# Performance work log

Measured on AMD Instinct MI355X. Metric: run time of the kernel, lower is better.

The kernel has to match this reference:

```python
import jax, jax.numpy as jnp
import numpy as np

B, N, D, H = 4, 2048, 512, 8
HEAD = D // H
TEMP = 8.0


def setup_inputs() -> dict:
    key = jax.random.key(0)
    k1, k2, k3, k4 = jax.random.split(key, 4)
    return {
        "keys": jax.random.normal(k1, (B, N, D), dtype=jnp.float32),
        "queries": jax.random.normal(k2, (B, N, D), dtype=jnp.float32),
        "values": jax.random.normal(k3, (B, N, D), dtype=jnp.float32),
        "W_comb": jax.random.normal(k4, (D, D), dtype=jnp.float32) * (1.0 / np.sqrt(D)),
        "b_comb": jnp.zeros((D,), dtype=jnp.float32),
    }


def reference(keys, queries, values, W_comb, b_comb):
    b, nk, d = keys.shape
    nq = queries.shape[1]
    h, hd = H, HEAD
    # split heads: (b, n, d) -> (b, n, h, hd)
    k = keys.reshape(b, nk, h, hd)
    q = queries.reshape(b, nq, h, hd)
    v = values.reshape(b, nk, h, hd)
    # scaled dot-product attention per head
    logits = jnp.einsum("bqhd,bkhd->bhqk", q, k) / TEMP  # (b, h, nq, nk)
    w = jax.nn.softmax(logits, axis=-1)
    out = jnp.einsum("bhqk,bkhd->bqhd", w, v).reshape(b, nq, d)
    # head_combine: Linear with bias (torch: x @ W.T + b)
    return out @ W_comb.T + b_comb
```

## Files before the change

kernel.cpp:

```cpp
#include <hip/hip_runtime.h>

#define B_ 4
#define N_ 2048
#define D_ 512
#define H_ 8

typedef __attribute__((ext_vector_type(8))) short bf16x8;
typedef __attribute__((ext_vector_type(4))) short bf16x4;
typedef __attribute__((ext_vector_type(4))) float f32x4;

#define KP 68

__device__ __forceinline__ unsigned short f32_to_bf16(float f) {
  unsigned int u = __float_as_uint(f);
  u += 0x7FFFu + ((u >> 16) & 1u);
  return (unsigned short)(u >> 16);
}

__device__ __forceinline__ unsigned int pack2_bf16(float a, float b) {
#if __has_builtin(__builtin_amdgcn_cvt_pk_bf16_f32)
  typedef __attribute__((ext_vector_type(2))) __bf16 bf16v2;
  bf16v2 r = __builtin_amdgcn_cvt_pk_bf16_f32(a, b);
  return *(unsigned int*)&r;
#else
  return (unsigned int)f32_to_bf16(a) | ((unsigned int)f32_to_bf16(b) << 16);
#endif
}

__device__ __forceinline__ float fast_exp2(float x) {
#if __has_builtin(__builtin_amdgcn_exp2f)
  return __builtin_amdgcn_exp2f(x);
#else
  return exp2f(x);
#endif
}

__device__ __forceinline__ f32x4 mfma16(bf16x4 a, bf16x4 b, f32x4 c) {
#if __has_builtin(__builtin_amdgcn_mfma_f32_16x16x16_bf16)
  return __builtin_amdgcn_mfma_f32_16x16x16_bf16(a, b, c, 0, 0, 0);
#else
  return __builtin_amdgcn_mfma_f32_16x16x16bf16_1k(a, b, c, 0, 0, 0);
#endif
}

__global__ __launch_bounds__(256) void convert_kernel(
    const float* __restrict__ Kf, const float* __restrict__ Qf,
    const float* __restrict__ Vf, const float* __restrict__ Wf,
    unsigned short* __restrict__ Qb, unsigned short* __restrict__ Kb,
    unsigned short* __restrict__ Wb, unsigned short* __restrict__ Vt) {
  __shared__ float tile[64 * 72];
  const int tid = threadIdx.x;
  if (blockIdx.x < 1024) {
    const float qs = 0.125f * 1.4426950408889634f;
    int gid = blockIdx.x * 256 + tid;
    const float4* Q4 = (const float4*)Qf;
    const float4* K4 = (const float4*)Kf;
    for (int i = gid; i < (B_ * N_ * D_) / 4; i += 262144) {
      float4 q = Q4[i];
      ((uint2*)Qb)[i] = make_uint2(pack2_bf16(q.x * qs, q.y * qs),
                                   pack2_bf16(q.z * qs, q.w * qs));
      float4 k = K4[i];
      ((uint2*)Kb)[i] = make_uint2(pack2_bf16(k.x, k.y), pack2_bf16(k.z, k.w));
    }
    if (gid < (D_ * D_) / 4) {
      float4 w = ((const float4*)Wf)[gid];
      ((uint2*)Wb)[gid] = make_uint2(pack2_bf16(w.x, w.y), pack2_bf16(w.z, w.w));
    }
  } else {
    int bid = blockIdx.x - 1024;
    int nt = bid & 31, bh = bid >> 5;
    int b = bh >> 3, h = bh & 7;
    int n0 = nt * 64;
#pragma unroll
    for (int i = 0; i < 4; ++i) {
      int idx = i * 256 + tid;
      int r = idx >> 4, c = idx & 15;
      *(float4*)&tile[r * 72 + c * 4] =
          *(const float4*)(Vf + (size_t)(b * N_ + n0 + r) * D_ + h * 64 + c * 4);
    }
    __syncthreads();
    int d = tid >> 2, c = tid & 3;
    unsigned int o[8];
#pragma unroll
    for (int j = 0; j < 8; ++j)
      o[j] = pack2_bf16(tile[(c * 16 + 2 * j) * 72 + d],
                        tile[(c * 16 + 2 * j + 1) * 72 + d]);
    unsigned short* dst = Vt + ((size_t)bh * 64 + d) * N_ + n0 + c * 16;
    *(bf16x8*)dst = *(bf16x8*)&o[0];
    *(bf16x8*)(dst + 8) = *(bf16x8*)&o[4];
  }
}

__global__ __launch_bounds__(256, 2) void attn_kernel(
    const unsigned short* __restrict__ Qb, const unsigned short* __restrict__ Kb,
    const unsigned short* __restrict__ Vt, unsigned short* __restrict__ Ob) {
  __shared__ unsigned short Kl[2][64 * KP];
  __shared__ unsigned short Vl[2][64 * KP];

  const int tid = threadIdx.x;
  const int w = tid >> 6;
  const int lane = tid & 63;
  const int lr = lane & 15;
  const int lq = lane >> 4;

  const int lid = blockIdx.y * gridDim.x + blockIdx.x;
  const int xcd = lid & 7;
  const int lin = lid >> 3;
  const int bh = xcd * 4 + (lin >> 4);
  const int qb = (lin & 15) * 128;

  const size_t slab = (size_t)(bh >> 3) * N_ * D_ + (size_t)(bh & 7) * 64;
  const unsigned short* kbase = Kb + slab;
  const unsigned short* vtbase = Vt + (size_t)bh * 64 * N_;

  bf16x8 qa[2][2];
#pragma unroll
  for (int g = 0; g < 2; ++g) {
    const unsigned short* qrow =
        Qb + slab + (size_t)(qb + w * 32 + g * 16 + lr) * D_;
    qa[g][0] = *(const bf16x8*)(qrow + 8 * lq);
    qa[g][1] = *(const bf16x8*)(qrow + 32 + 8 * lq);
  }

  f32x4 O[4][2];
#pragma unroll
  for (int i = 0; i < 4; ++i)
#pragma unroll
    for (int g = 0; g < 2; ++g) O[i][g] = (f32x4){0.f, 0.f, 0.f, 0.f};
  float l_g[2] = {0.f, 0.f};

  const int st_r = tid >> 3;
  const int st_c = tid & 7;

  {
    const unsigned short* ksrc = kbase + (size_t)st_r * D_ + st_c * 8;
    bf16x8 a = *(const bf16x8*)ksrc;
    bf16x8 b = *(const bf16x8*)(ksrc + (size_t)32 * D_);
    const unsigned short* vsrc = vtbase + (size_t)st_r * N_ + st_c * 8;
    bf16x8 c = *(const bf16x8*)vsrc;
    bf16x8 d = *(const bf16x8*)(vsrc + (size_t)32 * N_);
    *(bf16x8*)&Kl[0][st_r * KP + st_c * 8] = a;
    *(bf16x8*)&Kl[0][(st_r + 32) * KP + st_c * 8] = b;
    *(bf16x8*)&Vl[0][st_r * KP + st_c * 8] = c;
    *(bf16x8*)&Vl[0][(st_r + 32) * KP + st_c * 8] = d;
  }

  for (int kt = 0; kt < 32; ++kt) {
    const int p = kt & 1;
    __syncthreads();

    bf16x8 nk0, nk1, nv0, nv1;
    const bool more = (kt + 1) < 32;
    if (more) {
      const int kb1 = (kt + 1) * 64;
      const unsigned short* ksrc = kbase + (size_t)(kb1 + st_r) * D_ + st_c * 8;
      nk0 = *(const bf16x8*)ksrc;
      nk1 = *(const bf16x8*)(ksrc + (size_t)32 * D_);
      const unsigned short* vsrc = vtbase + (size_t)st_r * N_ + kb1 + st_c * 8;
      nv0 = *(const bf16x8*)vsrc;
      nv1 = *(const bf16x8*)(vsrc + (size_t)32 * N_);
    }

    f32x4 S[4][2];
#pragma unroll
    for (int nt = 0; nt < 4; ++nt) {
      bf16x8 kf0 = *(const bf16x8*)&Kl[p][(nt * 16 + lr) * KP + 8 * lq];
      bf16x8 kf1 = *(const bf16x8*)&Kl[p][(nt * 16 + lr) * KP + 32 + 8 * lq];
#pragma unroll
      for (int g = 0; g < 2; ++g) {
        S[nt][g] = __builtin_amdgcn_mfma_f32_16x16x32_bf16(
            kf0, qa[g][0], (f32x4){0.f, 0.f, 0.f, 0.f}, 0, 0, 0);
        S[nt][g] = __builtin_amdgcn_mfma_f32_16x16x32_bf16(kf1, qa[g][1],
                                                           S[nt][g], 0, 0, 0);
      }
    }

    bf16x4 pf[4][2];
#pragma unroll
    for (int nt = 0; nt < 4; ++nt)
#pragma unroll
      for (int g = 0; g < 2; ++g) {
        float p0 = fast_exp2(S[nt][g][0]);
        float p1 = fast_exp2(S[nt][g][1]);
        float p2 = fast_exp2(S[nt][g][2]);
        float p3 = fast_exp2(S[nt][g][3]);
        l_g[g] += (p0 + p1) + (p2 + p3);
        uint2 packed = make_uint2(pack2_bf16(p0, p1), pack2_bf16(p2, p3));
        pf[nt][g] = *(bf16x4*)&packed;
      }

#pragma unroll
    for (int dt = 0; dt < 4; ++dt) {
#pragma unroll
      for (int nt = 0; nt < 4; ++nt) {
        bf16x4 vf =
            *(const bf16x4*)&Vl[p][(dt * 16 + lr) * KP + nt * 16 + 4 * lq];
#pragma unroll
        for (int g = 0; g < 2; ++g)
          O[dt][g] = mfma16(vf, pf[nt][g], O[dt][g]);
      }
    }

    if (more) {
      *(bf16x8*)&Kl[1 - p][st_r * KP + st_c * 8] = nk0;
      *(bf16x8*)&Kl[1 - p][(st_r + 32) * KP + st_c * 8] = nk1;
      *(bf16x8*)&Vl[1 - p][st_r * KP + st_c * 8] = nv0;
      *(bf16x8*)&Vl[1 - p][(st_r + 32) * KP + st_c * 8] = nv1;
    }
  }

#pragma unroll
  for (int g = 0; g < 2; ++g) {
    l_g[g] += __shfl_xor(l_g[g], 16);
    l_g[g] += __shfl_xor(l_g[g], 32);
  }

  __syncthreads();
  unsigned short* SR = &Kl[0][0];
#pragma unroll
  for (int g = 0; g < 2; ++g) {
    float linv = 1.0f / l_g[g];
#pragma unroll
    for (int dt = 0; dt < 4; ++dt) {
      float v0 = O[dt][g][0] * linv;
      float v1 = O[dt][g][1] * linv;
      float v2 = O[dt][g][2] * linv;
      float v3 = O[dt][g][3] * linv;
      uint2 packed = make_uint2(pack2_bf16(v0, v1), pack2_bf16(v2, v3));
      *(bf16x4*)&SR[(w * 32 + g * 16 + lr) * KP + dt * 16 + lq * 4] =
          *(bf16x4*)&packed;
    }
  }
  __syncthreads();
  {
    const int row = tid >> 1, half = tid & 1;
    unsigned short* dst = Ob + slab + (size_t)(qb + row) * D_ + half * 32;
    const unsigned short* src = &SR[row * KP + half * 32];
    *(bf16x8*)dst = *(const bf16x8*)src;
    *(bf16x8*)(dst + 8) = *(const bf16x8*)(src + 8);
    *(bf16x8*)(dst + 16) = *(const bf16x8*)(src + 16);
    *(bf16x8*)(dst + 24) = *(const bf16x8*)(src + 24);
  }
}

#define GP 68
__global__ __launch_bounds__(256, 2) void gemm_kernel(
    const unsigned short* __restrict__ A, const unsigned short* __restrict__ Wb,
    const float* __restrict__ bias, float* __restrict__ out) {
  __shared__ unsigned short A_lds[2][64 * GP];
  __shared__ unsigned short W_lds[2][128 * GP];

  const int tid = threadIdx.x;
  const int w = tid >> 6;
  const int lane = tid & 63;
  const int lr = lane & 15;
  const int lq = lane >> 4;

  const int bid = blockIdx.x;
  const int xcd = bid & 7;
  const int lin = bid >> 3;
  const int mb = (xcd * 16 + (lin >> 2)) * 64;
  const int cb = (lin & 3) * 128;

  const int dc = (tid & 7) * 8;
  const int r0 = tid >> 3;

  f32x4 acc[8];
#pragma unroll
  for (int i = 0; i < 8; ++i) acc[i] = (f32x4){0.f, 0.f, 0.f, 0.f};

  {
    *(bf16x8*)&A_lds[0][r0 * GP + dc] =
        *(const bf16x8*)(A + (size_t)(mb + r0) * D_ + dc);
    *(bf16x8*)&A_lds[0][(r0 + 32) * GP + dc] =
        *(const bf16x8*)(A + (size_t)(mb + r0 + 32) * D_ + dc);
#pragma unroll
    for (int j = 0; j < 4; ++j)
      *(bf16x8*)&W_lds[0][(r0 + 32 * j) * GP + dc] =
          *(const bf16x8*)(Wb + (size_t)(cb + r0 + 32 * j) * D_ + dc);
  }

  for (int kt = 0; kt < 8; ++kt) {
    const int p = kt & 1;
    __syncthreads();

    bf16x8 na0, na1, nw0, nw1, nw2, nw3;
    const bool more = (kt + 1) < 8;
    if (more) {
      const int k1 = (kt + 1) * 64;
      na0 = *(const bf16x8*)(A + (size_t)(mb + r0) * D_ + k1 + dc);
      na1 = *(const bf16x8*)(A + (size_t)(mb + r0 + 32) * D_ + k1 + dc);
      nw0 = *(const bf16x8*)(Wb + (size_t)(cb + r0) * D_ + k1 + dc);
      nw1 = *(const bf16x8*)(Wb + (size_t)(cb + r0 + 32) * D_ + k1 + dc);
      nw2 = *(const bf16x8*)(Wb + (size_t)(cb + r0 + 64) * D_ + k1 + dc);
      nw3 = *(const bf16x8*)(Wb + (size_t)(cb + r0 + 96) * D_ + k1 + dc);
    }

    bf16x8 a0 = *(const bf16x8*)&A_lds[p][(w * 16 + lr) * GP + 8 * lq];
    bf16x8 a1 = *(const bf16x8*)&A_lds[p][(w * 16 + lr) * GP + 32 + 8 * lq];
#pragma unroll
    for (int nt = 0; nt < 8; ++nt) {
      bf16x8 b0 = *(const bf16x8*)&W_lds[p][(nt * 16 + lr) * GP + 8 * lq];
      bf16x8 b1 = *(const bf16x8*)&W_lds[p][(nt * 16 + lr) * GP + 32 + 8 * lq];
      acc[nt] = __builtin_amdgcn_mfma_f32_16x16x32_bf16(a0, b0, acc[nt], 0, 0, 0);
      acc[nt] = __builtin_amdgcn_mfma_f32_16x16x32_bf16(a1, b1, acc[nt], 0, 0, 0);
    }

    if (more) {
      *(bf16x8*)&A_lds[1 - p][r0 * GP + dc] = na0;
      *(bf16x8*)&A_lds[1 - p][(r0 + 32) * GP + dc] = na1;
      *(bf16x8*)&W_lds[1 - p][r0 * GP + dc] = nw0;
      *(bf16x8*)&W_lds[1 - p][(r0 + 32) * GP + dc] = nw1;
      *(bf16x8*)&W_lds[1 - p][(r0 + 64) * GP + dc] = nw2;
      *(bf16x8*)&W_lds[1 - p][(r0 + 96) * GP + dc] = nw3;
    }
  }

#pragma unroll
  for (int nt = 0; nt < 8; ++nt) {
    float bc = bias[cb + nt * 16 + lr];
#pragma unroll
    for (int rr = 0; rr < 4; ++rr) {
      int row = mb + w * 16 + lq * 4 + rr;
      out[(size_t)row * D_ + cb + nt * 16 + lr] = acc[nt][rr] + bc;
    }
  }
}

extern "C" void kernel_launch(void* const* d_in, const int* in_sizes, int n_in,
                              void* d_out, int out_size, void* d_ws,
                              size_t ws_size, hipStream_t stream) {
  (void)in_sizes; (void)n_in; (void)out_size; (void)ws_size;
  const float* keys    = (const float*)d_in[0];
  const float* queries = (const float*)d_in[1];
  const float* values  = (const float*)d_in[2];
  const float* W       = (const float*)d_in[3];
  const float* bias    = (const float*)d_in[4];
  float* out = (float*)d_out;

  char* ws = (char*)d_ws;
  unsigned short* Qb = (unsigned short*)(ws);
  unsigned short* Kb = (unsigned short*)(ws + 8388608);
  unsigned short* Vt = (unsigned short*)(ws + 16777216);
  unsigned short* Wb = (unsigned short*)(ws + 25165824);
  unsigned short* Ab = (unsigned short*)(ws + 25690112);

  convert_kernel<<<2048, 256, 0, stream>>>(keys, queries, values, W,
                                           Qb, Kb, Wb, Vt);

  attn_kernel<<<dim3(N_ / 128, B_ * H_), 256, 0, stream>>>(Qb, Kb, Vt, Ab);

  gemm_kernel<<<512, 256, 0, stream>>>(Ab, Wb, bias, out);
}
```

Before: 162.8 us.

## Fuse Q and W bf16 conversion into attention and GEMM kernels

Removes the separate Q and W fp32-to-bf16 conversion passes from the convert kernel. The attention kernel now loads fp32 queries and scales and converts them in registers, and the GEMM loads fp32 W tiles and converts them before storing to LDS. This cuts a full round trip of Q through the workspace, at the cost of wider fp32 loads in the consumers. The packing helper also drops the hardware packed-convert builtin in favour of software rounding.

Measured after the change: 163.7 us. Within noise of the previous version (+0.5%).

```diff
diff --git a/kernel.cpp b/kernel.cpp
--- a/kernel.cpp
+++ b/kernel.cpp
@@ -18,13 +18,16 @@
 }
 
 __device__ __forceinline__ unsigned int pack2_bf16(float a, float b) {
-#if __has_builtin(__builtin_amdgcn_cvt_pk_bf16_f32)
-  typedef __attribute__((ext_vector_type(2))) __bf16 bf16v2;
-  bf16v2 r = __builtin_amdgcn_cvt_pk_bf16_f32(a, b);
-  return *(unsigned int*)&r;
-#else
   return (unsigned int)f32_to_bf16(a) | ((unsigned int)f32_to_bf16(b) << 16);
-#endif
+}
+
+__device__ __forceinline__ bf16x8 cvt8_bf16(float4 a, float4 b, float s) {
+  union { unsigned int u[4]; bf16x8 v; } r;
+  r.u[0] = pack2_bf16(a.x * s, a.y * s);
+  r.u[1] = pack2_bf16(a.z * s, a.w * s);
+  r.u[2] = pack2_bf16(b.x * s, b.y * s);
+  r.u[3] = pack2_bf16(b.z * s, b.w * s);
+  return r.v;
 }
 
 __device__ __forceinline__ float fast_exp2(float x) {
@@ -44,27 +47,16 @@
 }
 
 __global__ __launch_bounds__(256) void convert_kernel(
-    const float* __restrict__ Kf, const float* __restrict__ Qf,
-    const float* __restrict__ Vf, const float* __restrict__ Wf,
-    unsigned short* __restrict__ Qb, unsigned short* __restrict__ Kb,
-    unsigned short* __restrict__ Wb, unsigned short* __restrict__ Vt) {
+    const float* __restrict__ Kf, const float* __restrict__ Vf,
+    unsigned short* __restrict__ Kb, unsigned short* __restrict__ Vt) {
   __shared__ float tile[64 * 72];
   const int tid = threadIdx.x;
   if (blockIdx.x < 1024) {
-    const float qs = 0.125f * 1.4426950408889634f;
     int gid = blockIdx.x * 256 + tid;
-    const float4* Q4 = (const float4*)Qf;
     const float4* K4 = (const float4*)Kf;
     for (int i = gid; i < (B_ * N_ * D_) / 4; i += 262144) {
-      float4 q = Q4[i];
-      ((uint2*)Qb)[i] = make_uint2(pack2_bf16(q.x * qs, q.y * qs),
-                                   pack2_bf16(q.z * qs, q.w * qs));
       float4 k = K4[i];
       ((uint2*)Kb)[i] = make_uint2(pack2_bf16(k.x, k.y), pack2_bf16(k.z, k.w));
-    }
-    if (gid < (D_ * D_) / 4) {
-      float4 w = ((const float4*)Wf)[gid];
-      ((uint2*)Wb)[gid] = make_uint2(pack2_bf16(w.x, w.y), pack2_bf16(w.z, w.w));
     }
   } else {
     int bid = blockIdx.x - 1024;
@@ -92,7 +84,7 @@
 }
 
 __global__ __launch_bounds__(256, 2) void attn_kernel(
-    const unsigned short* __restrict__ Qb, const unsigned short* __restrict__ Kb,
+    const float* __restrict__ Qf, const unsigned short* __restrict__ Kb,
     const unsigned short* __restrict__ Vt, unsigned short* __restrict__ Ob) {
   __shared__ unsigned short Kl[2][64 * KP];
   __shared__ unsigned short Vl[2][64 * KP];
@@ -114,12 +106,19 @@
   const unsigned short* vtbase = Vt + (size_t)bh * 64 * N_;
 
   bf16x8 qa[2][2];
-#pragma unroll
-  for (int g = 0; g < 2; ++g) {
-    const unsigned short* qrow =
-        Qb + slab + (size_t)(qb + w * 32 + g * 16 + lr) * D_;
-    qa[g][0] = *(const bf16x8*)(qrow + 8 * lq);
-    qa[g][1] = *(const bf16x8*)(qrow + 32 + 8 * lq);
+  {
+    const float qs = 0.125f * 1.4426950408889634f;
+#pragma unroll
+    for (int g = 0; g < 2; ++g) {
+      const float* qrow =
+          Qf + slab + (size_t)(qb + w * 32 + g * 16 + lr) * D_;
+      float4 a0 = *(const float4*)(qrow + 8 * lq);
+      float4 a1 = *(const float4*)(qrow + 8 * lq + 4);
+      qa[g][0] = cvt8_bf16(a0, a1, qs);
+      float4 b0 = *(const float4*)(qrow + 32 + 8 * lq);
+      float4 b1 = *(const float4*)(qrow + 36 + 8 * lq);
+      qa[g][1] = cvt8_bf16(b0, b1, qs);
+    }
   }
 
   f32x4 O[4][2];
@@ -245,7 +244,7 @@
 
 #define GP 68
 __global__ __launch_bounds__(256, 2) void gemm_kernel(
-    const unsigned short* __restrict__ A, const unsigned short* __restrict__ Wb,
+    const unsigned short* __restrict__ A, const float* __restrict__ Wf,
     const float* __restrict__ bias, float* __restrict__ out) {
   __shared__ unsigned short A_lds[2][64 * GP];
   __shared__ unsigned short W_lds[2][128 * GP];
@@ -275,25 +274,31 @@
     *(bf16x8*)&A_lds[0][(r0 + 32) * GP + dc] =
         *(const bf16x8*)(A + (size_t)(mb + r0 + 32) * D_ + dc);
 #pragma unroll
-    for (int j = 0; j < 4; ++j)
-      *(bf16x8*)&W_lds[0][(r0 + 32 * j) * GP + dc] =
-          *(const bf16x8*)(Wb + (size_t)(cb + r0 + 32 * j) * D_ + dc);
+    for (int j = 0; j < 4; ++j) {
+      const float* wsrc = Wf + (size_t)(cb + r0 + 32 * j) * D_ + dc;
+      float4 wa = *(const float4*)wsrc;
+      float4 wb = *(const float4*)(wsrc + 4);
+      *(bf16x8*)&W_lds[0][(r0 + 32 * j) * GP + dc] = cvt8_bf16(wa, wb, 1.0f);
+    }
   }
 
   for (int kt = 0; kt < 8; ++kt) {
     const int p = kt & 1;
     __syncthreads();
 
-    bf16x8 na0, na1, nw0, nw1, nw2, nw3;
+    bf16x8 na0, na1;
+    float4 nwA[4], nwB[4];
     const bool more = (kt + 1) < 8;
     if (more) {
       const int k1 = (kt + 1) * 64;
       na0 = *(const bf16x8*)(A + (size_t)(mb + r0) * D_ + k1 + dc);
       na1 = *(const bf16x8*)(A + (size_t)(mb + r0 + 32) * D_ + k1 + dc);
-      nw0 = *(const bf16x8*)(Wb + (size_t)(cb + r0) * D_ + k1 + dc);
-      nw1 = *(const bf16x8*)(Wb + (size_t)(cb + r0 + 32) * D_ + k1 + dc);
-      nw2 = *(const bf16x8*)(Wb + (size_t)(cb + r0 + 64) * D_ + k1 + dc);
-      nw3 = *(const bf16x8*)(Wb + (size_t)(cb + r0 + 96) * D_ + k1 + dc);
+#pragma unroll
+      for (int j = 0; j < 4; ++j) {
+        const float* wsrc = Wf + (size_t)(cb + r0 + 32 * j) * D_ + k1 + dc;
+        nwA[j] = *(const float4*)wsrc;
+        nwB[j] = *(const float4*)(wsrc + 4);
+      }
     }
 
     bf16x8 a0 = *(const bf16x8*)&A_lds[p][(w * 16 + lr) * GP + 8 * lq];
@@ -309,10 +314,10 @@
     if (more) {
       *(bf16x8*)&A_lds[1 - p][r0 * GP + dc] = na0;
       *(bf16x8*)&A_lds[1 - p][(r0 + 32) * GP + dc] = na1;
-      *(bf16x8*)&W_lds[1 - p][r0 * GP + dc] = nw0;
-      *(bf16x8*)&W_lds[1 - p][(r0 + 32) * GP + dc] = nw1;
-      *(bf16x8*)&W_lds[1 - p][(r0 + 64) * GP + dc] = nw2;
-      *(bf16x8*)&W_lds[1 - p][(r0 + 96) * GP + dc] = nw3;
+#pragma unroll
+      for (int j = 0; j < 4; ++j)
+        *(bf16x8*)&W_lds[1 - p][(r0 + 32 * j) * GP + dc] =
+            cvt8_bf16(nwA[j], nwB[j], 1.0f);
     }
   }
 
@@ -339,16 +344,13 @@
   float* out = (float*)d_out;
 
   char* ws = (char*)d_ws;
-  unsigned short* Qb = (unsigned short*)(ws);
   unsigned short* Kb = (unsigned short*)(ws + 8388608);
   unsigned short* Vt = (unsigned short*)(ws + 16777216);
-  unsigned short* Wb = (unsigned short*)(ws + 25165824);
   unsigned short* Ab = (unsigned short*)(ws + 25690112);
 
-  convert_kernel<<<2048, 256, 0, stream>>>(keys, queries, values, W,
-                                           Qb, Kb, Wb, Vt);
-
-  attn_kernel<<<dim3(N_ / 128, B_ * H_), 256, 0, stream>>>(Qb, Kb, Vt, Ab);
-
-  gemm_kernel<<<512, 256, 0, stream>>>(Ab, Wb, bias, out);
-}
+  convert_kernel<<<2048, 256, 0, stream>>>(keys, values, Kb, Vt);
+
+  attn_kernel<<<dim3(N_ / 128, B_ * H_), 256, 0, stream>>>(queries, Kb, Vt, Ab);
+
+  gemm_kernel<<<512, 256, 0, stream>>>(Ab, W, bias, out);
+}
```

## Halve attention block to two waves, each handling 64 query rows

Applied to the files above, without the earlier changes.

The attention kernel now launches 128 threads (two waves) per 128-query block instead of four. Each wave handles 64 query rows (four 16-row groups), so every K/V fragment read from LDS feeds twice as many MFMAs. Each thread now stages four rows of K and V per tile. The QK, exp and pack steps are also interleaved per group, which shortens the live range of the score registers. The trade-off is more registers per thread (larger O accumulators and Q fragments) and fewer waves per block to hide latency.

Result: slower. 201.6 us (+23.8%).

```diff
diff --git a/kernel.cpp b/kernel.cpp
--- a/kernel.cpp
+++ b/kernel.cpp
@@ -91,7 +91,7 @@
   }
 }
 
-__global__ __launch_bounds__(256, 2) void attn_kernel(
+__global__ __launch_bounds__(128, 2) void attn_kernel(
     const unsigned short* __restrict__ Qb, const unsigned short* __restrict__ Kb,
     const unsigned short* __restrict__ Vt, unsigned short* __restrict__ Ob) {
   __shared__ unsigned short Kl[2][64 * KP];
@@ -113,81 +113,71 @@
   const unsigned short* kbase = Kb + slab;
   const unsigned short* vtbase = Vt + (size_t)bh * 64 * N_;
 
-  bf16x8 qa[2][2];
-#pragma unroll
-  for (int g = 0; g < 2; ++g) {
+  bf16x8 qa[4][2];
+#pragma unroll
+  for (int g = 0; g < 4; ++g) {
     const unsigned short* qrow =
-        Qb + slab + (size_t)(qb + w * 32 + g * 16 + lr) * D_;
+        Qb + slab + (size_t)(qb + w * 64 + g * 16 + lr) * D_;
     qa[g][0] = *(const bf16x8*)(qrow + 8 * lq);
     qa[g][1] = *(const bf16x8*)(qrow + 32 + 8 * lq);
   }
 
-  f32x4 O[4][2];
+  f32x4 O[4][4];
 #pragma unroll
   for (int i = 0; i < 4; ++i)
 #pragma unroll
-    for (int g = 0; g < 2; ++g) O[i][g] = (f32x4){0.f, 0.f, 0.f, 0.f};
-  float l_g[2] = {0.f, 0.f};
+    for (int g = 0; g < 4; ++g) O[i][g] = (f32x4){0.f, 0.f, 0.f, 0.f};
+  float l_g[4] = {0.f, 0.f, 0.f, 0.f};
 
   const int st_r = tid >> 3;
   const int st_c = tid & 7;
 
   {
-    const unsigned short* ksrc = kbase + (size_t)st_r * D_ + st_c * 8;
-    bf16x8 a = *(const bf16x8*)ksrc;
-    bf16x8 b = *(const bf16x8*)(ksrc + (size_t)32 * D_);
-    const unsigned short* vsrc = vtbase + (size_t)st_r * N_ + st_c * 8;
-    bf16x8 c = *(const bf16x8*)vsrc;
-    bf16x8 d = *(const bf16x8*)(vsrc + (size_t)32 * N_);
-    *(bf16x8*)&Kl[0][st_r * KP + st_c * 8] = a;
-    *(bf16x8*)&Kl[0][(st_r + 32) * KP + st_c * 8] = b;
-    *(bf16x8*)&Vl[0][st_r * KP + st_c * 8] = c;
-    *(bf16x8*)&Vl[0][(st_r + 32) * KP + st_c * 8] = d;
+#pragma unroll
+    for (int j = 0; j < 4; ++j) {
+      const int r = st_r + 16 * j;
+      bf16x8 a = *(const bf16x8*)(kbase + (size_t)r * D_ + st_c * 8);
+      bf16x8 c = *(const bf16x8*)(vtbase + (size_t)r * N_ + st_c * 8);
+      *(bf16x8*)&Kl[0][r * KP + st_c * 8] = a;
+      *(bf16x8*)&Vl[0][r * KP + st_c * 8] = c;
+    }
   }
 
   for (int kt = 0; kt < 32; ++kt) {
     const int p = kt & 1;
     __syncthreads();
 
-    bf16x8 nk0, nk1, nv0, nv1;
+    bf16x8 nk[4], nv[4];
     const bool more = (kt + 1) < 32;
     if (more) {
       const int kb1 = (kt + 1) * 64;
-      const unsigned short* ksrc = kbase + (size_t)(kb1 + st_r) * D_ + st_c * 8;
-      nk0 = *(const bf16x8*)ksrc;
-      nk1 = *(const bf16x8*)(ksrc + (size_t)32 * D_);
-      const unsigned short* vsrc = vtbase + (size_t)st_r * N_ + kb1 + st_c * 8;
-      nv0 = *(const bf16x8*)vsrc;
-      nv1 = *(const bf16x8*)(vsrc + (size_t)32 * N_);
-    }
-
-    f32x4 S[4][2];
+#pragma unroll
+      for (int j = 0; j < 4; ++j) {
+        const int r = st_r + 16 * j;
+        nk[j] = *(const bf16x8*)(kbase + (size_t)(kb1 + r) * D_ + st_c * 8);
+        nv[j] = *(const bf16x8*)(vtbase + (size_t)r * N_ + kb1 + st_c * 8);
+      }
+    }
+
+    bf16x4 pf[4][4];
 #pragma unroll
     for (int nt = 0; nt < 4; ++nt) {
       bf16x8 kf0 = *(const bf16x8*)&Kl[p][(nt * 16 + lr) * KP + 8 * lq];
       bf16x8 kf1 = *(const bf16x8*)&Kl[p][(nt * 16 + lr) * KP + 32 + 8 * lq];
 #pragma unroll
-      for (int g = 0; g < 2; ++g) {
-        S[nt][g] = __builtin_amdgcn_mfma_f32_16x16x32_bf16(
+      for (int g = 0; g < 4; ++g) {
+        f32x4 S = __builtin_amdgcn_mfma_f32_16x16x32_bf16(
             kf0, qa[g][0], (f32x4){0.f, 0.f, 0.f, 0.f}, 0, 0, 0);
-        S[nt][g] = __builtin_amdgcn_mfma_f32_16x16x32_bf16(kf1, qa[g][1],
-                                                           S[nt][g], 0, 0, 0);
-      }
-    }
-
-    bf16x4 pf[4][2];
-#pragma unroll
-    for (int nt = 0; nt < 4; ++nt)
-#pragma unroll
-      for (int g = 0; g < 2; ++g) {
-        float p0 = fast_exp2(S[nt][g][0]);
-        float p1 = fast_exp2(S[nt][g][1]);
-        float p2 = fast_exp2(S[nt][g][2]);
-        float p3 = fast_exp2(S[nt][g][3]);
+        S = __builtin_amdgcn_mfma_f32_16x16x32_bf16(kf1, qa[g][1], S, 0, 0, 0);
+        float p0 = fast_exp2(S[0]);
+        float p1 = fast_exp2(S[1]);
+        float p2 = fast_exp2(S[2]);
+        float p3 = fast_exp2(S[3]);
         l_g[g] += (p0 + p1) + (p2 + p3);
         uint2 packed = make_uint2(pack2_bf16(p0, p1), pack2_bf16(p2, p3));
         pf[nt][g] = *(bf16x4*)&packed;
       }
+    }
 
 #pragma unroll
     for (int dt = 0; dt < 4; ++dt) {
@@ -196,21 +186,23 @@
         bf16x4 vf =
             *(const bf16x4*)&Vl[p][(dt * 16 + lr) * KP + nt * 16 + 4 * lq];
 #pragma unroll
-        for (int g = 0; g < 2; ++g)
+        for (int g = 0; g < 4; ++g)
           O[dt][g] = mfma16(vf, pf[nt][g], O[dt][g]);
       }
     }
 
     if (more) {
-      *(bf16x8*)&Kl[1 - p][st_r * KP + st_c * 8] = nk0;
-      *(bf16x8*)&Kl[1 - p][(st_r + 32) * KP + st_c * 8] = nk1;
-      *(bf16x8*)&Vl[1 - p][st_r * KP + st_c * 8] = nv0;
-      *(bf16x8*)&Vl[1 - p][(st_r + 32) * KP + st_c * 8] = nv1;
-    }
-  }
-
-#pragma unroll
-  for (int g = 0; g < 2; ++g) {
+#pragma unroll
+      for (int j = 0; j < 4; ++j) {
+        const int r = st_r + 16 * j;
+        *(bf16x8*)&Kl[1 - p][r * KP + st_c * 8] = nk[j];
+        *(bf16x8*)&Vl[1 - p][r * KP + st_c * 8] = nv[j];
+      }
+    }
+  }
+
+#pragma unroll
+  for (int g = 0; g < 4; ++g) {
     l_g[g] += __shfl_xor(l_g[g], 16);
     l_g[g] += __shfl_xor(l_g[g], 32);
   }
@@ -218,7 +210,7 @@
   __syncthreads();
   unsigned short* SR = &Kl[0][0];
 #pragma unroll
-  for (int g = 0; g < 2; ++g) {
+  for (int g = 0; g < 4; ++g) {
     float linv = 1.0f / l_g[g];
 #pragma unroll
     for (int dt = 0; dt < 4; ++dt) {
@@ -227,19 +219,22 @@
       float v2 = O[dt][g][2] * linv;
       float v3 = O[dt][g][3] * linv;
       uint2 packed = make_uint2(pack2_bf16(v0, v1), pack2_bf16(v2, v3));
-      *(bf16x4*)&SR[(w * 32 + g * 16 + lr) * KP + dt * 16 + lq * 4] =
+      *(bf16x4*)&SR[(w * 64 + g * 16 + lr) * KP + dt * 16 + lq * 4] =
           *(bf16x4*)&packed;
     }
   }
   __syncthreads();
   {
-    const int row = tid >> 1, half = tid & 1;
-    unsigned short* dst = Ob + slab + (size_t)(qb + row) * D_ + half * 32;
-    const unsigned short* src = &SR[row * KP + half * 32];
+    unsigned short* dst = Ob + slab + (size_t)(qb + tid) * D_;
+    const unsigned short* src = &SR[tid * KP];
     *(bf16x8*)dst = *(const bf16x8*)src;
+    *(bf16x8*)(dst + 16) = *(const bf16x8*)(src + 16);
+    *(bf16x8*)(dst + 32) = *(const bf16x8*)(src + 32);
+    *(bf16x8*)(dst + 48) = *(const bf16x8*)(src + 48);
     *(bf16x8*)(dst + 8) = *(const bf16x8*)(src + 8);
-    *(bf16x8*)(dst + 16) = *(const bf16x8*)(src + 16);
     *(bf16x8*)(dst + 24) = *(const bf16x8*)(src + 24);
+    *(bf16x8*)(dst + 40) = *(const bf16x8*)(src + 40);
+    *(bf16x8*)(dst + 56) = *(const bf16x8*)(src + 56);
   }
 }
 
@@ -348,7 +343,7 @@
   convert_kernel<<<2048, 256, 0, stream>>>(keys, queries, values, W,
                                            Qb, Kb, Wb, Vt);
 
-  attn_kernel<<<dim3(N_ / 128, B_ * H_), 256, 0, stream>>>(Qb, Kb, Vt, Ab);
+  attn_kernel<<<dim3(N_ / 128, B_ * H_), 128, 0, stream>>>(Qb, Kb, Vt, Ab);
 
   gemm_kernel<<<512, 256, 0, stream>>>(Ab, Wb, bias, out);
 }
```
